# Kernel tuning notes

Measured on AMD Instinct MI355X. Metric: run time of the kernel, lower is better.

## Reference

```python
import jax, jax.numpy as jnp
import numpy as np

N = 4096          # number of real POIs (distance_matrix is [N, N])
D = 64            # poi_dim
B = 8             # users (samples)
DAYS = 4          # days per user
L = 64            # POI ids per day
SCALE = 50.0      # max distance -> arange(0, 50+0.5, 0.5) = 101 bucket boundaries
NUM_INTERVALS = 101


def setup_inputs() -> dict:
    key = jax.random.key(0)
    k1, k2, k3 = jax.random.split(key, 3)
    poi_weight = jax.random.normal(k1, (N + 1, D), dtype=jnp.float32)
    distance_matrix = jax.random.uniform(k2, (N, N), dtype=jnp.float32) * SCALE
    # POI ids in [1, N]: no padding zeros, so lastDay[lastDay != 0] == lastDay (static shape)
    seqInDay = jax.random.randint(k3, (B * DAYS, L), 1, N + 1)
    sampleIdOfDay_set = jnp.repeat(jnp.arange(B), DAYS)
    return {
        "poi_weight": poi_weight,
        "distance_matrix": distance_matrix,
        "seqInDay": seqInDay,
        "sampleIdOfDay_set": sampleIdOfDay_set,
        "GCN_layer_num": 2,
    }


def reference(poi_weight, distance_matrix, seqInDay, sampleIdOfDay_set, GCN_layer_num):
    # group days by sample id (stable sort == torch sorted+groupby); equal group sizes
    ids = np.asarray(sampleIdOfDay_set)
    order = np.argsort(ids, kind="stable")
    nb = int(np.unique(ids).size)
    days = ids.shape[0] // nb
    samples = seqInDay[order].reshape(nb, days, -1)            # [B, days, L]

    poi_emb = poi_weight[1:]                                    # [N, D]
    intervals = jnp.arange(0.0, SCALE + 0.5, 0.5)               # [NUM_INTERVALS]
    # bucket of every distance entry under the torch mask rule:
    # intervals[i-1] <= d < intervals[i]  <=>  searchsorted(side='right')
    dm_bucket = jnp.searchsorted(intervals, distance_matrix, side="right")  # [N, N] int
    diag = jnp.arange(distance_matrix.shape[0])
    scale = jnp.sqrt(jnp.float32(poi_weight.shape[1]))

    def per_sample(sample):                                     # sample: [days, L]
        lastDay = sample[-1]                                    # all ids nonzero
        spans = distance_matrix[lastDay[:-1] - 1, lastDay[1:] - 1]
        # torch.bucketize(right=False) == searchsorted side='left'
        span_idx = jnp.searchsorted(intervals, spans, side="left")
        w = jnp.bincount(span_idx, length=NUM_INTERVALS).astype(jnp.float32)
        w = w / w.sum()
        # buckets actually visited by this sample (torch loops over unique())
        present = jnp.zeros(NUM_INTERVALS, dtype=bool).at[span_idx].set(True)
        W = jnp.where(present[dm_bucket], w[dm_bucket], 0.0)    # [N, N]
        W = W.at[diag, diag].set(1.0)                            # fill_diagonal_(1)
        deg = jnp.maximum(jnp.sqrt(W.sum(-1, keepdims=True)), 1e-12)
        adj = W / deg / deg.T                                    # D^-1/2 A D^-1/2
        out = poi_emb
        layer = poi_emb
        for _ in range(GCN_layer_num):
            layer = jnp.tanh(adj @ layer)
            out = out + layer                                    # sum over stacked layers
        table = jnp.concatenate([poi_weight[:1], out], axis=0)  # [N+1, D]
        return table[sample] * scale                             # [days, L, D]

    res = jax.vmap(per_sample)(samples)                          # [B, days, L, D]
    return res.reshape(nb * days, samples.shape[-1], -1)
```

## Files before the change

### kernel.cpp

```cpp
#include <hip/hip_runtime.h>
#include <hip/hip_bf16.h>
#include <math.h>

typedef __bf16 bf16x8 __attribute__((ext_vector_type(8)));
typedef float  f32x4  __attribute__((ext_vector_type(4)));
typedef unsigned short ushort_t;
typedef unsigned char  u8;
typedef unsigned int   u32;

#define N_POI 4096
#define NB    8
#define NDAYS 4
#define LSEQ  64
#define NROWS 32
#define NBINS 102
#define KC    6

static __device__ __forceinline__ u32 bf16bits(float f) {
  u32 x = __float_as_uint(f);
  return ((x + 0x7FFFu + ((x >> 16) & 1u)) >> 16) & 0xFFFFu;
}

static __device__ __forceinline__ float b2f(ushort_t u) {
  return __uint_as_float((u32)u << 16);
}

static __device__ __forceinline__ void gload16(void* lds, const void* g) {
  __builtin_amdgcn_global_load_lds(
      (const __attribute__((address_space(1))) u32*)g,
      (__attribute__((address_space(3))) u32*)lds, 16, 0, 0);
}

__global__ __launch_bounds__(64) void k_sample(const int* __restrict__ ids,
                                               const int* __restrict__ seq,
                                               const float* __restrict__ dm,
                                               float* __restrict__ tfp,
                                               u32* __restrict__ tbu,
                                               int* __restrict__ meta) {
  __shared__ int sh_ids[NROWS];
  __shared__ int sh_order[NROWS];
  __shared__ int sh_cnt[NBINS];
  __shared__ int sh_last[LSEQ];
  __shared__ int sh_nb;
  const int tid = threadIdx.x, s = blockIdx.x;
  if (tid < NROWS) sh_ids[tid] = ids[tid];
  for (int k = tid; k < NBINS; k += 64) sh_cnt[k] = 0;
  if (tid == 0) sh_nb = 0;
  __syncthreads();
  if (tid < NROWS) {
    const int my = sh_ids[tid];
    int rank = 0, first = 1;
    for (int j = 0; j < NROWS; ++j) {
      const int v = sh_ids[j];
      if (v < my || (v == my && j < tid)) rank++;
      if (v == my && j < tid) first = 0;
    }
    sh_order[rank] = tid;
    if (first) atomicAdd(&sh_nb, 1);
  }
  __syncthreads();
  const int nb = sh_nb;
  const int days = NROWS / nb;
  if (s == 0) {
    if (tid < NROWS) meta[tid] = sh_order[tid];
    if (tid == 0) meta[NROWS] = days;
  }
  const int lastRow = sh_order[s * days + days - 1];
  sh_last[tid] = seq[lastRow * LSEQ + tid];
  __syncthreads();
  if (tid < LSEQ - 1) {
    const float v = dm[(size_t)(sh_last[tid] - 1) * N_POI + (sh_last[tid + 1] - 1)];
    int si = (int)ceilf(2.0f * v);
    si = min(max(si, 0), 101);
    atomicAdd(&sh_cnt[si], 1);
  }
  __syncthreads();
  const float inv = 1.0f / (float)(LSEQ - 1);
  for (int k = tid; k < 128; k += 64) {
    const float wv = (k < NBINS) ? (float)sh_cnt[k] * inv : 0.0f;
    tfp[s * 128 + k] = wv;
    tbu[s * 128 + k] = bf16bits(wv);
  }
}

__global__ __launch_bounds__(256) void k_bucket(const float* __restrict__ dm,
                                                const float* __restrict__ tfp,
                                                u8* __restrict__ bucket,
                                                float* __restrict__ rbuf) {
  const int row = blockIdx.x, tid = threadIdx.x;
  __shared__ int h[2][NBINS];
  __shared__ float tl[NB][NBINS];
  __shared__ int sh_bii;
  for (int k = tid; k < 2 * NBINS; k += 256) ((int*)h)[k] = 0;
  __syncthreads();
  const float4* drow = (const float4*)(dm + (size_t)row * N_POI);
  u32* brow = (u32*)(bucket + (size_t)row * N_POI);
  int* hp = h[tid >> 7];
  const int jdiag = row >> 2;
  for (int it = 0; it < 4; ++it) {
    const int j = it * 256 + tid;
    const float4 v = drow[j];
    const int b0 = min((int)(2.0f * v.x) + 1, 101);
    const int b1 = min((int)(2.0f * v.y) + 1, 101);
    const int b2 = min((int)(2.0f * v.z) + 1, 101);
    const int b3 = min((int)(2.0f * v.w) + 1, 101);
    atomicAdd(&hp[b0], 1); atomicAdd(&hp[b1], 1);
    atomicAdd(&hp[b2], 1); atomicAdd(&hp[b3], 1);
    const u32 pk = (u32)b0 | ((u32)b1 << 8) | ((u32)b2 << 16) | ((u32)b3 << 24);
    if (j == jdiag) sh_bii = (int)((pk >> (8 * (row & 3))) & 255u);
    brow[j] = pk;
  }
  for (int idx = tid; idx < NB * NBINS; idx += 256)
    tl[idx / NBINS][idx % NBINS] = tfp[(idx / NBINS) * 128 + (idx % NBINS)];
  __syncthreads();
  for (int k = tid; k < NBINS; k += 256) h[0][k] += h[1][k];
  __syncthreads();
  const int s = tid >> 5, ln = tid & 31;
  float dot = 0.f;
  for (int k = ln; k < NBINS; k += 32) dot += (float)h[0][k] * tl[s][k];
#pragma unroll
  for (int off = 16; off >= 1; off >>= 1) dot += __shfl_down(dot, off, 32);
  if (ln == 0) {
    const float ri = rsqrtf(dot - tl[s][sh_bii] + 1.0f);
    rbuf[s * N_POI + row] = ri;
  }
}

__global__ __launch_bounds__(256) void k_rows(const float* __restrict__ rbuf,
                                              const float* __restrict__ poi,
                                              ushort_t* __restrict__ y1t) {
  const int s = blockIdx.y;
  const int i = blockIdx.x * 256 + threadIdx.x;
  const float ri = rbuf[s * N_POI + i];
#pragma unroll 8
  for (int d = 0; d < 64; ++d) {
    const float pv = poi[(size_t)(i + 1) * 64 + d];
    y1t[((size_t)s * 64 + d) * N_POI + i] = (ushort_t)bf16bits(ri * pv);
  }
}

__global__ __launch_bounds__(256, 3) void k_layer(
    const u8* __restrict__ bucket, const u32* __restrict__ tbu,
    const ushort_t* __restrict__ yin, ushort_t* __restrict__ part) {
  const int rb = blockIdx.x, kc = blockIdx.y, g = blockIdx.z;
  const int s0 = 2 * g, s1 = 2 * g + 1;
  const int tid = threadIdx.x;
  const int lane = tid & 63, w = tid >> 6;
  const int loff = tid & 31;

  __shared__ u32 trep[NBINS * 32];
  __shared__ ushort_t Ybuf[2][2][64 * 64];

  const int gi0 = rb * 128;
  const int r0 = gi0 + w * 32 + (lane & 15);
  const u8* brow0 = bucket + (size_t)r0 * N_POI;
  const u8* brow1 = brow0 + (size_t)16 * N_POI;
  const int kq = (lane >> 4) * 8;

  const ushort_t* ybase0 = yin + (size_t)s0 * 64 * N_POI;
  const ushort_t* ybase1 = yin + (size_t)s1 * 64 * N_POI;

  const int d0s = tid >> 3, d1s = 32 + d0s;
  const int bly = (tid & 7) * 16;
  const int sw0 = bly ^ (((d0s & 7) ^ ((d0s >> 3) & 1)) << 4);
  const int sw1 = bly ^ (((d1s & 7) ^ ((d1s >> 3) & 1)) << 4);
  const char* g00 = (const char*)(ybase0 + (size_t)d0s * N_POI) + sw0;
  const char* g01 = (const char*)(ybase0 + (size_t)d1s * N_POI) + sw1;
  const char* g10 = (const char*)(ybase1 + (size_t)d0s * N_POI) + sw0;
  const char* g11 = (const char*)(ybase1 + (size_t)d1s * N_POI) + sw1;

  const int kt0 = (kc * 64) / KC, kt1 = ((kc + 1) * 64) / KC;

  uint2 bpA[4], bpB[4];

#define LOADB_(dst, ktv)                                   \
  {                                                        \
    const int _kb = (ktv) * 64;                            \
    dst[0] = *(const uint2*)(brow0 + _kb + kq);            \
    dst[1] = *(const uint2*)(brow0 + _kb + 32 + kq);       \
    dst[2] = *(const uint2*)(brow1 + _kb + kq);            \
    dst[3] = *(const uint2*)(brow1 + _kb + 32 + kq);       \
  }

#define STAGE_(bufi, ktv)                                  \
  {                                                        \
    const size_t _kb = (size_t)(ktv) * 128;                \
    char* _lb = (char*)&Ybuf[bufi][0][0] + tid * 16;       \
    gload16(_lb, g00 + _kb);                               \
    gload16(_lb + 4096, g01 + _kb);                        \
    gload16(_lb + 8192, g10 + _kb);                        \
    gload16(_lb + 12288, g11 + _kb);                       \
  }

  STAGE_(0, kt0);
  LOADB_(bpA, kt0);
  for (int idx = tid; idx < NBINS * 32; idx += 256) {
    const int b = idx >> 5;
    trep[idx] = tbu[s0 * 128 + b] | (tbu[s1 * 128 + b] << 16);
  }

  f32x4 acc0[2][4], acc1[2][4];
#pragma unroll
  for (int mt = 0; mt < 2; ++mt)
#pragma unroll
    for (int nt = 0; nt < 4; ++nt) {
      acc0[mt][nt] = (f32x4){0.f, 0.f, 0.f, 0.f};
      acc1[mt][nt] = (f32x4){0.f, 0.f, 0.f, 0.f};
    }

  asm volatile("s_waitcnt vmcnt(0)" ::: "memory");
  __syncthreads();

#define BODY_(CB, PB, CUR)                                                     \
  {                                                                            \
    const int k0 = kt * 64;                                                    \
    if (kt + 1 < kt1) { STAGE_((CUR) ^ 1, kt + 1); LOADB_(PB, kt + 1); }       \
    bf16x8 af0[2][2], af1[2][2];                                               \
    _Pragma("unroll") for (int mt = 0; mt < 2; ++mt) {                         \
      _Pragma("unroll") for (int ks = 0; ks < 2; ++ks) {                       \
        const uint2 bb = CB[mt * 2 + ks];                                      \
        u32 tv[8];                                                             \
        _Pragma("unroll") for (int e = 0; e < 4; ++e) tv[e] =                  \
            trep[((bb.x >> (8 * e)) & 255u) * 32 + loff];                      \
        _Pragma("unroll") for (int e = 0; e < 4; ++e) tv[4 + e] =              \
            trep[((bb.y >> (8 * e)) & 255u) * 32 + loff];                      \
        const u32 de = (u32)(r0 + mt * 16 - (k0 + ks * 32 + kq));              \
        if (de < 8u) {             \
          _Pragma("unroll") for (int e = 0; e < 8; ++e)                        \
              if (de == (u32)e) tv[e] = 0x3F803F80u;                           \
        }                                                                      \
        uint4 p0, p1;                                                          \
        p0.x = (tv[0] & 0xFFFFu) | (tv[1] << 16);                              \
        p0.y = (tv[2] & 0xFFFFu) | (tv[3] << 16);                              \
        p0.z = (tv[4] & 0xFFFFu) | (tv[5] << 16);                              \
        p0.w = (tv[6] & 0xFFFFu) | (tv[7] << 16);                              \
        p1.x = (tv[0] >> 16) | (tv[1] & 0xFFFF0000u);                          \
        p1.y = (tv[2] >> 16) | (tv[3] & 0xFFFF0000u);                          \
        p1.z = (tv[4] >> 16) | (tv[5] & 0xFFFF0000u);                          \
        p1.w = (tv[6] >> 16) | (tv[7] & 0xFFFF0000u);                          \
        union { uint4 u; bf16x8 v; } c0, c1;                                   \
        c0.u = p0; c1.u = p1;                                                  \
        af0[mt][ks] = c0.v; af1[mt][ks] = c1.v;                                \
      }                                                                        \
    }                                                                          \
    const char* _y0 = (const char*)&Ybuf[CUR][0][0];                           \
    const char* _y1 = (const char*)&Ybuf[CUR][1][0];                           \
    _Pragma("unroll") for (int ks = 0; ks < 2; ++ks) {                         \
      _Pragma("unroll") for (int nt = 0; nt < 4; ++nt) {                       \
        const int rY = nt * 16 + (lane & 15);                                  \
        const int pm = (rY & 7) ^ ((rY >> 3) & 1);                             \
        const int la = rY * 128 + (((ks * 4 + (lane >> 4)) ^ pm) << 4);        \
        union { uint4 u; bf16x8 v; } b0, b1;                                   \
        b0.u = *(const uint4*)(_y0 + la);                                      \
        b1.u = *(const uint4*)(_y1 + la);                                      \
        acc0[0][nt] = __builtin_amdgcn_mfma_f32_16x16x32_bf16(af0[0][ks], b0.v, \
                                                              acc0[0][nt], 0, 0, 0); \
        acc0[1][nt] = __builtin_amdgcn_mfma_f32_16x16x32_bf16(af0[1][ks], b0.v, \
                                                              acc0[1][nt], 0, 0, 0); \
        acc1[0][nt] = __builtin_amdgcn_mfma_f32_16x16x32_bf16(af1[0][ks], b1.v, \
                                                              acc1[0][nt], 0, 0, 0); \
        acc1[1][nt] = __builtin_amdgcn_mfma_f32_16x16x32_bf16(af1[1][ks], b1.v, \
                                                              acc1[1][nt], 0, 0, 0); \
      }                                                                        \
    }                                                                          \
    asm volatile("s_waitcnt vmcnt(0)" ::: "memory");                           \
    __syncthreads();      \
  }

  int kt = kt0;
  while (true) {
    BODY_(bpA, bpB, 0);
    if (++kt >= kt1) break;
    BODY_(bpB, bpA, 1);
    if (++kt >= kt1) break;
  }

#undef BODY_
#undef STAGE_
#undef LOADB_

#pragma unroll
  for (int mt = 0; mt < 2; ++mt) {
#pragma unroll
    for (int e = 0; e < 4; ++e) {
      const int row = gi0 + w * 32 + mt * 16 + (lane >> 4) * 4 + e;
#pragma unroll
      for (int nt = 0; nt < 4; ++nt) {
        const int col = nt * 16 + (lane & 15);
        part[(((size_t)kc * NB + s0) * N_POI + row) * 64 + col] =
            (ushort_t)bf16bits(acc0[mt][nt][e]);
        part[(((size_t)kc * NB + s1) * N_POI + row) * 64 + col] =
            (ushort_t)bf16bits(acc1[mt][nt][e]);
      }
    }
  }
}

__global__ __launch_bounds__(256) void k_reduce(
    const ushort_t* __restrict__ part, const float* __restrict__ rbuf,
    const float* __restrict__ poi, float* __restrict__ table,
    ushort_t* __restrict__ y2t) {
  const int it = blockIdx.x, s = blockIdx.y, tid = threadIdx.x;
  __shared__ ushort_t Tt[64 * 72];
#pragma unroll
  for (int j = 0; j < 2; ++j) {
    const int s2 = tid + j * 256;
    const int iloc = s2 >> 3, d0 = (s2 & 7) * 8;
    const int i = it * 64 + iloc;
    const size_t po = ((size_t)s * N_POI + i) * 64 + d0;
    float x[8] = {0.f, 0.f, 0.f, 0.f, 0.f, 0.f, 0.f, 0.f};
#pragma unroll
    for (int c = 0; c < KC; ++c) {
      uint4 p = *(const uint4*)(part + (size_t)c * NB * N_POI * 64 + po);
      const u32* a = (const u32*)&p;
#pragma unroll
      for (int q = 0; q < 4; ++q) {
        x[2 * q]     += __uint_as_float(a[q] << 16);
        x[2 * q + 1] += __uint_as_float(a[q] & 0xFFFF0000u);
      }
    }
    const float ri = rbuf[s * N_POI + i];
    float t[8];
#pragma unroll
    for (int e = 0; e < 8; ++e) t[e] = tanhf(ri * x[e]);
    float* trow = table + po;
    const float* prow = poi + (size_t)(i + 1) * 64 + d0;
    float4 pz0 = *(const float4*)prow;
    float4 pz1 = *(const float4*)(prow + 4);
    float4 o0 = {pz0.x + t[0], pz0.y + t[1], pz0.z + t[2], pz0.w + t[3]};
    float4 o1 = {pz1.x + t[4], pz1.y + t[5], pz1.z + t[6], pz1.w + t[7]};
    *(float4*)trow = o0;
    *(float4*)(trow + 4) = o1;
#pragma unroll
    for (int e = 0; e < 8; ++e)
      Tt[(d0 + e) * 72 + iloc] = (ushort_t)bf16bits(ri * t[e]);
  }
  __syncthreads();
  const int d = tid >> 2, i0 = (tid & 3) * 16;
  uint4 a = *(const uint4*)&Tt[d * 72 + i0];
  uint4 b = *(const uint4*)&Tt[d * 72 + i0 + 8];
  ushort_t* dst = y2t + ((size_t)s * 64 + d) * N_POI + it * 64 + i0;
  *(uint4*)dst = a;
  *(uint4*)(dst + 8) = b;
}

__global__ __launch_bounds__(256) void k_gather(const int* __restrict__ seq,
                                                const int* __restrict__ meta,
                                                const float* __restrict__ table,
                                                const float* __restrict__ poi,
                                                const ushort_t* __restrict__ part,
                                                const float* __restrict__ rbuf,
                                                float* __restrict__ out) {
  const int r = blockIdx.x;
  const int p = blockIdx.y * 4 + (threadIdx.x >> 6);
  const int d = threadIdx.x & 63;
  const int days = meta[NROWS];
  const int srcrow = meta[r];
  const int g = r / days;
  const int id = seq[srcrow * LSEQ + p];
  float v;
  if (id == 0) {
    v = poi[d];
  } else {
    const size_t po = ((size_t)g * N_POI + (id - 1)) * 64 + d;
    float x2 = 0.f;
#pragma unroll
    for (int c = 0; c < KC; ++c)
      x2 += b2f(part[(size_t)c * NB * N_POI * 64 + po]);
    v = table[po] + tanhf(rbuf[g * N_POI + (id - 1)] * x2);
  }
  out[((size_t)r * LSEQ + p) * 64 + d] = v * 8.0f;
}

extern "C" void kernel_launch(void* const* d_in, const int* in_sizes, int n_in,
                              void* d_out, int out_size, void* d_ws, size_t ws_size,
                              hipStream_t stream) {
  (void)in_sizes; (void)n_in; (void)out_size; (void)ws_size;
  const float* poi = (const float*)d_in[0];
  const float* dm  = (const float*)d_in[1];
  const int*   seq = (const int*)d_in[2];
  const int*   ids = (const int*)d_in[3];

  char* ws = (char*)d_ws;
  size_t off = 0;
  auto carve = [&](size_t bytes) {
    char* p = ws + off;
    off += (bytes + 255) & ~(size_t)255;
    return p;
  };
  u8*       bucket = (u8*)carve((size_t)N_POI * N_POI);
  float*    tfp    = (float*)carve((size_t)NB * 128 * 4);
  u32*      tbu    = (u32*)carve((size_t)NB * 128 * 4);
  float*    rbuf   = (float*)carve((size_t)NB * N_POI * 4);
  float*    table  = (float*)carve((size_t)NB * N_POI * 64 * 4);
  ushort_t* y1t    = (ushort_t*)table;
  ushort_t* y2t    = (ushort_t*)carve((size_t)NB * 64 * N_POI * 2);
  ushort_t* part   = (ushort_t*)carve((size_t)KC * NB * N_POI * 64 * 2);
  int*      meta   = (int*)carve(256);

  k_sample<<<NB, 64, 0, stream>>>(ids, seq, dm, tfp, tbu, meta);
  k_bucket<<<N_POI, 256, 0, stream>>>(dm, tfp, bucket, rbuf);
  k_rows<<<dim3(16, NB), 256, 0, stream>>>(rbuf, poi, y1t);
  k_layer<<<dim3(32, KC, 4), 256, 0, stream>>>(bucket, tbu, y1t, part);
  k_reduce<<<dim3(64, NB), 256, 0, stream>>>(part, rbuf, poi, table, y2t);
  k_layer<<<dim3(32, KC, 4), 256, 0, stream>>>(bucket, tbu, y2t, part);
  k_gather<<<dim3(NROWS, 16), 256, 0, stream>>>(seq, meta, table, poi, part, rbuf,
                                                (float*)d_out);
}
```

Measured before the change: 185.2 us.

## Interleave paired-sample partials in u32 layout and widen histogram and row loads

k_layer now packs the bf16 partial results of the two samples it handles into one 32-bit word, so each store writes both samples with a single coalesced access instead of two scattered 16-bit writes. k_reduce and k_gather are reworked to read this interleaved layout, with k_reduce handling one sample pair per block. k_bucket spreads its LDS histogram over four copies instead of two to cut atomic contention, and k_rows reads poi rows as float4. The trade-off is half as many k_reduce blocks, each doing twice the work, and a strided 2-byte access pattern in the gather.

```diff
diff --git a/kernel.cpp b/kernel.cpp
--- a/kernel.cpp
+++ b/kernel.cpp
@@ -10,6 +10,7 @@
 
 #define N_POI 4096
 #define NB    8
+#define NPAIR 4
 #define NDAYS 4
 #define LSEQ  64
 #define NROWS 32
@@ -21,8 +22,11 @@
   return ((x + 0x7FFFu + ((x >> 16) & 1u)) >> 16) & 0xFFFFu;
 }
 
-static __device__ __forceinline__ float b2f(ushort_t u) {
-  return __uint_as_float((u32)u << 16);
+static __device__ __forceinline__ float lo16f(u32 v) {
+  return __uint_as_float(v << 16);
+}
+static __device__ __forceinline__ float hi16f(u32 v) {
+  return __uint_as_float(v & 0xFFFF0000u);
 }
 
 static __device__ __forceinline__ void gload16(void* lds, const void* g) {
@@ -88,14 +92,14 @@
                                                 u8* __restrict__ bucket,
                                                 float* __restrict__ rbuf) {
   const int row = blockIdx.x, tid = threadIdx.x;
-  __shared__ int h[2][NBINS];
+  __shared__ int h[4][NBINS];
   __shared__ float tl[NB][NBINS];
   __shared__ int sh_bii;
-  for (int k = tid; k < 2 * NBINS; k += 256) ((int*)h)[k] = 0;
+  for (int k = tid; k < 4 * NBINS; k += 256) ((int*)h)[k] = 0;
   __syncthreads();
   const float4* drow = (const float4*)(dm + (size_t)row * N_POI);
   u32* brow = (u32*)(bucket + (size_t)row * N_POI);
-  int* hp = h[tid >> 7];
+  int* hp = h[tid >> 6];
   const int jdiag = row >> 2;
   for (int it = 0; it < 4; ++it) {
     const int j = it * 256 + tid;
@@ -113,7 +117,8 @@
   for (int idx = tid; idx < NB * NBINS; idx += 256)
     tl[idx / NBINS][idx % NBINS] = tfp[(idx / NBINS) * 128 + (idx % NBINS)];
   __syncthreads();
-  for (int k = tid; k < NBINS; k += 256) h[0][k] += h[1][k];
+  for (int k = tid; k < NBINS; k += 256)
+    h[0][k] += h[1][k] + h[2][k] + h[3][k];
   __syncthreads();
   const int s = tid >> 5, ln = tid & 31;
   float dot = 0.f;
@@ -132,16 +137,21 @@
   const int s = blockIdx.y;
   const int i = blockIdx.x * 256 + threadIdx.x;
   const float ri = rbuf[s * N_POI + i];
-#pragma unroll 8
-  for (int d = 0; d < 64; ++d) {
-    const float pv = poi[(size_t)(i + 1) * 64 + d];
-    y1t[((size_t)s * 64 + d) * N_POI + i] = (ushort_t)bf16bits(ri * pv);
+  const float4* prow = (const float4*)(poi + (size_t)(i + 1) * 64);
+  ushort_t* dst = y1t + (size_t)s * 64 * N_POI + i;
+#pragma unroll
+  for (int q = 0; q < 16; ++q) {
+    const float4 v = prow[q];
+    dst[(size_t)(4 * q + 0) * N_POI] = (ushort_t)bf16bits(ri * v.x);
+    dst[(size_t)(4 * q + 1) * N_POI] = (ushort_t)bf16bits(ri * v.y);
+    dst[(size_t)(4 * q + 2) * N_POI] = (ushort_t)bf16bits(ri * v.z);
+    dst[(size_t)(4 * q + 3) * N_POI] = (ushort_t)bf16bits(ri * v.w);
   }
 }
 
 __global__ __launch_bounds__(256, 3) void k_layer(
     const u8* __restrict__ bucket, const u32* __restrict__ tbu,
-    const ushort_t* __restrict__ yin, ushort_t* __restrict__ part) {
+    const ushort_t* __restrict__ yin, u32* __restrict__ part) {
   const int rb = blockIdx.x, kc = blockIdx.y, g = blockIdx.z;
   const int s0 = 2 * g, s1 = 2 * g + 1;
   const int tid = threadIdx.x;
@@ -287,68 +297,83 @@
 #pragma unroll
       for (int nt = 0; nt < 4; ++nt) {
         const int col = nt * 16 + (lane & 15);
-        part[(((size_t)kc * NB + s0) * N_POI + row) * 64 + col] =
-            (ushort_t)bf16bits(acc0[mt][nt][e]);
-        part[(((size_t)kc * NB + s1) * N_POI + row) * 64 + col] =
-            (ushort_t)bf16bits(acc1[mt][nt][e]);
+        part[(((size_t)kc * NPAIR + g) * N_POI + row) * 64 + col] =
+            bf16bits(acc0[mt][nt][e]) | (bf16bits(acc1[mt][nt][e]) << 16);
       }
     }
   }
 }
 
 __global__ __launch_bounds__(256) void k_reduce(
-    const ushort_t* __restrict__ part, const float* __restrict__ rbuf,
+    const u32* __restrict__ part, const float* __restrict__ rbuf,
     const float* __restrict__ poi, float* __restrict__ table,
     ushort_t* __restrict__ y2t) {
-  const int it = blockIdx.x, s = blockIdx.y, tid = threadIdx.x;
-  __shared__ ushort_t Tt[64 * 72];
+  const int it = blockIdx.x, g = blockIdx.y, tid = threadIdx.x;
+  const int s0 = 2 * g, s1 = 2 * g + 1;
+  __shared__ ushort_t Tt[2][64 * 72];
 #pragma unroll
   for (int j = 0; j < 2; ++j) {
     const int s2 = tid + j * 256;
     const int iloc = s2 >> 3, d0 = (s2 & 7) * 8;
     const int i = it * 64 + iloc;
-    const size_t po = ((size_t)s * N_POI + i) * 64 + d0;
-    float x[8] = {0.f, 0.f, 0.f, 0.f, 0.f, 0.f, 0.f, 0.f};
+    const size_t po = ((size_t)g * N_POI + i) * 64 + d0;
+    float x0[8] = {0.f, 0.f, 0.f, 0.f, 0.f, 0.f, 0.f, 0.f};
+    float x1[8] = {0.f, 0.f, 0.f, 0.f, 0.f, 0.f, 0.f, 0.f};
 #pragma unroll
     for (int c = 0; c < KC; ++c) {
-      uint4 p = *(const uint4*)(part + (size_t)c * NB * N_POI * 64 + po);
-      const u32* a = (const u32*)&p;
+      const u32* sp = part + (size_t)c * NPAIR * N_POI * 64;
+      uint4 a = *(const uint4*)(sp + po);
+      uint4 b = *(const uint4*)(sp + po + 4);
+      const u32* au = (const u32*)&a;
+      const u32* bu = (const u32*)&b;
 #pragma unroll
       for (int q = 0; q < 4; ++q) {
-        x[2 * q]     += __uint_as_float(a[q] << 16);
-        x[2 * q + 1] += __uint_as_float(a[q] & 0xFFFF0000u);
+        x0[q] += lo16f(au[q]);     x1[q] += hi16f(au[q]);
+        x0[4 + q] += lo16f(bu[q]); x1[4 + q] += hi16f(bu[q]);
       }
     }
-    const float ri = rbuf[s * N_POI + i];
-    float t[8];
-#pragma unroll
-    for (int e = 0; e < 8; ++e) t[e] = tanhf(ri * x[e]);
-    float* trow = table + po;
+    const float r0 = rbuf[s0 * N_POI + i];
+    const float r1 = rbuf[s1 * N_POI + i];
+    float t0[8], t1[8];
+#pragma unroll
+    for (int e = 0; e < 8; ++e) { t0[e] = tanhf(r0 * x0[e]); t1[e] = tanhf(r1 * x1[e]); }
     const float* prow = poi + (size_t)(i + 1) * 64 + d0;
     float4 pz0 = *(const float4*)prow;
     float4 pz1 = *(const float4*)(prow + 4);
-    float4 o0 = {pz0.x + t[0], pz0.y + t[1], pz0.z + t[2], pz0.w + t[3]};
-    float4 o1 = {pz1.x + t[4], pz1.y + t[5], pz1.z + t[6], pz1.w + t[7]};
-    *(float4*)trow = o0;
-    *(float4*)(trow + 4) = o1;
-#pragma unroll
-    for (int e = 0; e < 8; ++e)
-      Tt[(d0 + e) * 72 + iloc] = (ushort_t)bf16bits(ri * t[e]);
+    float* trow0 = table + ((size_t)s0 * N_POI + i) * 64 + d0;
+    float* trow1 = table + ((size_t)s1 * N_POI + i) * 64 + d0;
+    float4 o;
+    o = (float4){pz0.x + t0[0], pz0.y + t0[1], pz0.z + t0[2], pz0.w + t0[3]};
+    *(float4*)trow0 = o;
+    o = (float4){pz1.x + t0[4], pz1.y + t0[5], pz1.z + t0[6], pz1.w + t0[7]};
+    *(float4*)(trow0 + 4) = o;
+    o = (float4){pz0.x + t1[0], pz0.y + t1[1], pz0.z + t1[2], pz0.w + t1[3]};
+    *(float4*)trow1 = o;
+    o = (float4){pz1.x + t1[4], pz1.y + t1[5], pz1.z + t1[6], pz1.w + t1[7]};
+    *(float4*)(trow1 + 4) = o;
+#pragma unroll
+    for (int e = 0; e < 8; ++e) {
+      Tt[0][(d0 + e) * 72 + iloc] = (ushort_t)bf16bits(r0 * t0[e]);
+      Tt[1][(d0 + e) * 72 + iloc] = (ushort_t)bf16bits(r1 * t1[e]);
+    }
   }
   __syncthreads();
   const int d = tid >> 2, i0 = (tid & 3) * 16;
-  uint4 a = *(const uint4*)&Tt[d * 72 + i0];
-  uint4 b = *(const uint4*)&Tt[d * 72 + i0 + 8];
-  ushort_t* dst = y2t + ((size_t)s * 64 + d) * N_POI + it * 64 + i0;
-  *(uint4*)dst = a;
-  *(uint4*)(dst + 8) = b;
+#pragma unroll
+  for (int ps = 0; ps < 2; ++ps) {
+    uint4 a = *(const uint4*)&Tt[ps][d * 72 + i0];
+    uint4 b = *(const uint4*)&Tt[ps][d * 72 + i0 + 8];
+    ushort_t* dst = y2t + ((size_t)(2 * g + ps) * 64 + d) * N_POI + it * 64 + i0;
+    *(uint4*)dst = a;
+    *(uint4*)(dst + 8) = b;
+  }
 }
 
 __global__ __launch_bounds__(256) void k_gather(const int* __restrict__ seq,
                                                 const int* __restrict__ meta,
                                                 const float* __restrict__ table,
                                                 const float* __restrict__ poi,
-                                                const ushort_t* __restrict__ part,
+                                                const u32* __restrict__ part,
                                                 const float* __restrict__ rbuf,
                                                 float* __restrict__ out) {
   const int r = blockIdx.x;
@@ -356,18 +381,21 @@
   const int d = threadIdx.x & 63;
   const int days = meta[NROWS];
   const int srcrow = meta[r];
-  const int g = r / days;
+  const int s = r / days;
   const int id = seq[srcrow * LSEQ + p];
   float v;
   if (id == 0) {
     v = poi[d];
   } else {
-    const size_t po = ((size_t)g * N_POI + (id - 1)) * 64 + d;
+    const size_t po = (((size_t)(s >> 1)) * N_POI + (id - 1)) * 64 + d;
     float x2 = 0.f;
 #pragma unroll
-    for (int c = 0; c < KC; ++c)
-      x2 += b2f(part[(size_t)c * NB * N_POI * 64 + po]);
-    v = table[po] + tanhf(rbuf[g * N_POI + (id - 1)] * x2);
+    for (int c = 0; c < KC; ++c) {
+      const u32 w = part[(size_t)c * NPAIR * N_POI * 64 + po];
+      x2 += (s & 1) ? hi16f(w) : lo16f(w);
+    }
+    v = table[((size_t)s * N_POI + (id - 1)) * 64 + d] +
+        tanhf(rbuf[s * N_POI + (id - 1)] * x2);
   }
   out[((size_t)r * LSEQ + p) * 64 + d] = v * 8.0f;
 }
@@ -395,15 +423,15 @@
   float*    table  = (float*)carve((size_t)NB * N_POI * 64 * 4);
   ushort_t* y1t    = (ushort_t*)table;
   ushort_t* y2t    = (ushort_t*)carve((size_t)NB * 64 * N_POI * 2);
-  ushort_t* part   = (ushort_t*)carve((size_t)KC * NB * N_POI * 64 * 2);
+  u32*      part   = (u32*)carve((size_t)KC * NPAIR * N_POI * 64 * 4);
   int*      meta   = (int*)carve(256);
 
   k_sample<<<NB, 64, 0, stream>>>(ids, seq, dm, tfp, tbu, meta);
   k_bucket<<<N_POI, 256, 0, stream>>>(dm, tfp, bucket, rbuf);
   k_rows<<<dim3(16, NB), 256, 0, stream>>>(rbuf, poi, y1t);
-  k_layer<<<dim3(32, KC, 4), 256, 0, stream>>>(bucket, tbu, y1t, part);
-  k_reduce<<<dim3(64, NB), 256, 0, stream>>>(part, rbuf, poi, table, y2t);
-  k_layer<<<dim3(32, KC, 4), 256, 0, stream>>>(bucket, tbu, y2t, part);
+  k_layer<<<dim3(32, KC, NPAIR), 256, 0, stream>>>(bucket, tbu, y1t, part);
+  k_reduce<<<dim3(64, NPAIR), 256, 0, stream>>>(part, rbuf, poi, table, y2t);
+  k_layer<<<dim3(32, KC, NPAIR), 256, 0, stream>>>(bucket, tbu, y2t, part);
   k_gather<<<dim3(NROWS, 16), 256, 0, stream>>>(seq, meta, table, poi, part, rbuf,
                                                 (float*)d_out);
 }
```

After: 187.0 us. Within noise of the previous version (+0.9%).
